# Performance work log

Hardware: AMD Instinct MI355X
Metric: run time of the kernel (lower is better)

The kernel has to match this reference:

```python
import jax, jax.numpy as jnp
import numpy as np

N = 2048      # feature_num (nodes/sensors)
T = 5         # timd_num (window length)
D = 64        # embed_dim
TOPK = 21     # topk + 1 (includes self, cos(i,i)=1)
B = 32        # batch
EPS = 1e-5
NEG_SLOPE = 0.2


def setup_inputs() -> dict:
    key = jax.random.key(0)
    ks = jax.random.split(key, 9)
    s = 1.0 / np.sqrt(D)
    return {
        "x": jax.random.normal(ks[0], (B, N, T), jnp.float32),
        "emb": jax.random.normal(ks[1], (N, D), jnp.float32) * s,      # embedding table
        "W": jax.random.normal(ks[2], (D, T), jnp.float32) * (1.0 / np.sqrt(T)),  # GNN lin weight
        "Wb": jax.random.normal(ks[3], (D,), jnp.float32) * 0.01,       # GNN lin bias
        "a_src": jax.random.normal(ks[4], (2 * D,), jnp.float32) * s,   # attention vec (source half)
        "a_dst": jax.random.normal(ks[5], (2 * D,), jnp.float32) * s,   # attention vec (dest half)
        "gamma": jnp.ones((D,), jnp.float32),                            # BatchNorm1d weight
        "beta": jnp.zeros((D,), jnp.float32),                            # BatchNorm1d bias
        "fc_w": jax.random.normal(ks[6], (1, D), jnp.float32) * s,      # fc weight
        "fc_b": jnp.zeros((1,), jnp.float32),                            # fc bias
    }


def reference(x, emb, W, Wb, a_src, a_dst, gamma, beta, fc_w, fc_b):
    # --- cosine-sim topk graph build ---
    norm = jnp.linalg.norm(emb, axis=-1)                    # [N]
    cos = (emb @ emb.T) / (norm[:, None] * norm[None, :])   # [N,N]
    _, idx = jax.lax.top_k(cos, TOPK)                       # [N,TOPK]
    # scatter one-hot adjacency (vectorized, no per-row loop)
    adj = jnp.zeros((N, N), x.dtype).at[jnp.arange(N)[:, None], idx].set(1.0)
    # --- GNN: GDN-style attention message passing ---
    h = jnp.einsum('bnt,dt->bnd', x, W) + Wb                # [B,N,D]
    g = jnp.concatenate([h, jnp.broadcast_to(emb, h.shape)], axis=-1)  # [B,N,2D]
    e_src = g @ a_src                                       # [B,N]
    e_dst = g @ a_dst                                       # [B,N]
    e = jax.nn.leaky_relu(e_src[:, :, None] + e_dst[:, None, :], NEG_SLOPE)  # [B,N,N]
    e = jnp.where(adj > 0, e, jnp.float32(-1e9))
    alpha = jax.nn.softmax(e, axis=-1)                      # [B,N,N], rows sum to 1 over TOPK nbrs
    z = jax.nn.relu(jnp.einsum('bij,bjd->bid', alpha, h))   # [B,N,D]
    # --- output head: z * emb, BN over channels, relu, fc ---
    out = z * emb                                           # [B,N,D]
    mean = out.mean(axis=(0, 1))                            # BN1d stats over (batch, nodes)
    var = out.var(axis=(0, 1))
    out = (out - mean) * jax.lax.rsqrt(var + EPS) * gamma + beta
    out = jax.nn.relu(out)
    out = out @ fc_w.T + fc_b                               # [B,N,1]
    return out.reshape(-1, N)                               # [B,N]
```

## Files before the change

### kernel.cpp

```cpp
#include <hip/hip_runtime.h>
#include <hip/hip_fp16.h>
#include <math.h>

#define N_NODES 2048
#define T_WIN 5
#define D_EMB 64
#define TOPK 21
#define B_BATCH 32
#define BN_TOTAL (B_BATCH * N_NODES)
#define EPS_BN 1e-5f
#define NEG_SLOPE 0.2f
#define STATS_STRIDE 16

typedef unsigned long long u64;
typedef unsigned short u16;
typedef unsigned int u32;

__device__ __forceinline__ float wave_sum(float v) {
#pragma unroll
    for (int off = 32; off > 0; off >>= 1) v += __shfl_xor(v, off, 64);
    return v;
}

__device__ __forceinline__ u64 max64(u64 a, u64 b) { return a > b ? a : b; }
__device__ __forceinline__ u64 min64(u64 a, u64 b) { return a < b ? a : b; }

__device__ __forceinline__ u64 bitonic_sort64_desc(u64 key, int lane) {
#pragma unroll
    for (int k = 2; k <= 64; k <<= 1) {
#pragma unroll
        for (int j = k >> 1; j >= 1; j >>= 1) {
            u64 pk = __shfl_xor(key, j, 64);
            bool dirDesc = ((lane & k) == 0);
            bool keepMax = (((lane & j) == 0) == dirDesc);
            key = keepMax ? max64(key, pk) : min64(key, pk);
        }
    }
    return key;
}

__device__ __forceinline__ u64 bitonic_merge_top64(u64 a, u64 b, int lane) {
    u64 br = __shfl(b, 63 - lane, 64);
    u64 c = max64(a, br);
#pragma unroll
    for (int j = 32; j >= 1; j >>= 1) {
        u64 pk = __shfl_xor(c, j, 64);
        bool keepMax = ((lane & j) == 0);
        c = keepMax ? max64(c, pk) : min64(c, pk);
    }
    return c;
}

__device__ __forceinline__ u16 f2bf(float f) {
    unsigned u = __float_as_uint(f);
    return (u16)((u + 0x7FFFu + ((u >> 16) & 1u)) >> 16);
}
__device__ __forceinline__ float bf2f(u16 h) {
    return __uint_as_float((unsigned)h << 16);
}

__global__ __launch_bounds__(256) void k_preg(
    const float* __restrict__ x, const float* __restrict__ W,
    const float* __restrict__ Wb, const float* __restrict__ a_src,
    const float* __restrict__ a_dst, const float* __restrict__ emb,
    float* __restrict__ xs2T, float* __restrict__ xd2T,
    float* __restrict__ es_embP, float* __restrict__ ed_embP,
    float* __restrict__ norms, float* __restrict__ dotM,
    float* __restrict__ stats, float* __restrict__ stats2) {
    __shared__ __align__(16) float As[64][68];
    __shared__ __align__(16) float Bs[64][68];
    int t = threadIdx.x;

    if (blockIdx.x >= 528) {
        int eb = blockIdx.x - 528;
        if (eb < 512) {
            if (eb < 2) {
                float* p = eb ? stats2 : stats;
                ((float4*)p)[t] = make_float4(0.f, 0.f, 0.f, 0.f);
            }
            int wid = t >> 6, lane = t & 63;
            int node = eb * 4 + wid;
            float e = emb[node * D_EMB + lane];
            float s2 = wave_sum(e * e);
            float esE = wave_sum(e * a_src[D_EMB + lane]);
            float edE = wave_sum(e * a_dst[D_EMB + lane]);
            if (lane == 0) {
                norms[node] = sqrtf(s2);
                es_embP[node] = esE;
                ed_embP[node] = edE;
            }
        } else {
            __shared__ float cws[5], cwd[5], cbs[2];
            if (t < 12) {
                int which = (t < 5 || t == 10) ? 0 : 1;
                const float* av = which ? a_dst : a_src;
                const float* sp;
                int stride;
                if (t < 10) { int tt = (t < 5) ? t : t - 5; sp = W + tt; stride = T_WIN; }
                else        { sp = Wb; stride = 1; }
                float acc = 0.f;
                for (int d = 0; d < D_EMB; d++) acc += sp[d * stride] * av[d];
                if (t < 5)       cws[t] = acc;
                else if (t < 10) cwd[t - 5] = acc;
                else             cbs[t - 10] = acc;
            }
            __syncthreads();
            float ws0 = cws[0], ws1 = cws[1], ws2 = cws[2], ws3 = cws[3], ws4 = cws[4];
            float wd0 = cwd[0], wd1 = cwd[1], wd2 = cwd[2], wd3 = cwd[3], wd4 = cwd[4];
            float bss = cbs[0], bsd = cbs[1];
            int base = (eb - 512) * 1024;
#pragma unroll
            for (int r = 0; r < 4; r++) {
                int item = base + 256 * r + t;
                const float* xp = x + (size_t)item * T_WIN;
                float x0 = xp[0], x1 = xp[1], x2 = xp[2], x3 = xp[3], x4 = xp[4];
                xs2T[item] = bss + x0 * ws0 + x1 * ws1 + x2 * ws2 + x3 * ws3 + x4 * ws4;
                xd2T[item] = bsd + x0 * wd0 + x1 * wd1 + x2 * wd2 + x3 * wd3 + x4 * wd4;
            }
        }
        return;
    }

    int g = blockIdx.x;
    int a = (int)((sqrtf(8.f * g + 1.f) - 1.f) * 0.5f);
    while ((a + 1) * (a + 2) / 2 <= g) a++;
    while (a * (a + 1) / 2 > g) a--;
    int bq = g - a * (a + 1) / 2;
    int i0 = a * 64, j0 = bq * 64;

    {
        int r = t >> 2, c0 = t & 3;
        const float4* srcA = (const float4*)(emb + (size_t)(i0 + r) * D_EMB);
        const float4* srcB = (const float4*)(emb + (size_t)(j0 + r) * D_EMB);
#pragma unroll
        for (int k = 0; k < 4; k++) {
            int f4 = c0 + 4 * k;
            float4 v = srcA[f4];
            int d = 4 * f4;
            As[d][r] = v.x; As[d + 1][r] = v.y; As[d + 2][r] = v.z; As[d + 3][r] = v.w;
            float4 w = srcB[f4];
            Bs[d][r] = w.x; Bs[d + 1][r] = w.y; Bs[d + 2][r] = w.z; Bs[d + 3][r] = w.w;
        }
    }
    __syncthreads();

    int ti = t & 15, tj = t >> 4;
    float acc[4][4] = {};
#pragma unroll
    for (int d = 0; d < 64; d++) {
        float4 av = *(const float4*)&As[d][4 * ti];
        float4 bv = *(const float4*)&Bs[d][4 * tj];
        acc[0][0] += av.x * bv.x; acc[0][1] += av.x * bv.y; acc[0][2] += av.x * bv.z; acc[0][3] += av.x * bv.w;
        acc[1][0] += av.y * bv.x; acc[1][1] += av.y * bv.y; acc[1][2] += av.y * bv.z; acc[1][3] += av.y * bv.w;
        acc[2][0] += av.z * bv.x; acc[2][1] += av.z * bv.y; acc[2][2] += av.z * bv.z; acc[2][3] += av.z * bv.w;
        acc[3][0] += av.w * bv.x; acc[3][1] += av.w * bv.y; acc[3][2] += av.w * bv.z; acc[3][3] += av.w * bv.w;
    }

#pragma unroll
    for (int r = 0; r < 4; r++) {
        float4 o;
        o.x = acc[r][0]; o.y = acc[r][1]; o.z = acc[r][2]; o.w = acc[r][3];
        int i = i0 + 4 * ti + r;
        *(float4*)(dotM + (size_t)i * N_NODES + j0 + 4 * tj) = o;
        dotM[(size_t)(j0 + 4 * tj + 0) * N_NODES + i] = o.x;
        dotM[(size_t)(j0 + 4 * tj + 1) * N_NODES + i] = o.y;
        dotM[(size_t)(j0 + 4 * tj + 2) * N_NODES + i] = o.z;
        dotM[(size_t)(j0 + 4 * tj + 3) * N_NODES + i] = o.w;
    }
}

__global__ __launch_bounds__(256) void k_select(
    const float* __restrict__ dotM, const float* __restrict__ norms,
    int* __restrict__ idxT) {
    __shared__ u64 candbuf[4][128];
    __shared__ u64 mbuf[2][64];
    int tid = threadIdx.x;
    int wid = tid >> 6, lane = tid & 63;
    int pair = wid >> 1;
    int half = wid & 1;
    int i = blockIdx.x * 2 + pair;
    int jbase = half * (N_NODES / 2);
    const float* row = dotM + (size_t)i * N_NODES + jbase;
    u64* buf = candbuf[wid];
    float ni = norms[i];

    u64 a = 0;
    u64 t = 0;
    int cnt = 0;
    float vcur = row[lane];
    float ncur = norms[jbase + lane];

#pragma unroll 1
    for (int c = 0; c < N_NODES / 128; c++) {
        int j = c * 64 + lane;
        float dv = vcur, nv = ncur;
        if (c < N_NODES / 128 - 1) {
            vcur = row[j + 64];
            ncur = norms[jbase + j + 64];
        }
        float v = dv / (ni * nv);
        unsigned u = __float_as_uint(v);
        u = (u & 0x80000000u) ? ~u : (u | 0x80000000u);
        u64 key = ((u64)u << 32) | (unsigned)(~(j + jbase));
        unsigned long long ball = __ballot(key > t);
        if (ball) {
            int ofs = __popcll(ball & ((1ull << lane) - 1ull));
            if (key > t) buf[cnt + ofs] = key;
            cnt += (int)__popcll(ball);
            if (cnt >= 64) {
                u64 nk = buf[lane];
                nk = bitonic_sort64_desc(nk, lane);
                a = bitonic_merge_top64(a, nk, lane);
                t = __shfl(a, 20, 64);
                int rem = cnt - 64;
                u64 mv = (lane < rem) ? buf[64 + lane] : 0;
                if (lane < rem) buf[lane] = mv;
                cnt = rem;
            }
        }
    }
    while (cnt > 0) {
        int take = cnt < 64 ? cnt : 64;
        u64 nk = (lane < take) ? buf[lane] : 0;
        nk = bitonic_sort64_desc(nk, lane);
        a = bitonic_merge_top64(a, nk, lane);
        t = __shfl(a, 20, 64);
        int rem = cnt - take;
        u64 mv = (lane < rem) ? buf[take + lane] : 0;
        if (lane < rem) buf[lane] = mv;
        cnt = rem;
    }

    if (half) mbuf[pair][lane] = a;
    __syncthreads();
    if (!half) {
        u64 bv = mbuf[pair][lane];
        a = bitonic_merge_top64(a, bv, lane);
        if (lane < TOPK) idxT[lane * N_NODES + i] = (int)(~(unsigned)a);
    }
}

__global__ __launch_bounds__(256) void k_alpha(
    const int* __restrict__ idxT, const float* __restrict__ xs2T,
    const float* __restrict__ xd2T, const float* __restrict__ es_embP,
    const float* __restrict__ ed_embP, u32* __restrict__ paT) {
    __shared__ float sed[N_NODES];
    int g = blockIdx.x;
    int b = g & 31;
    int i0 = (g >> 5) * 256;
    int t = threadIdx.x;

    {
        const float4* sxd = (const float4*)(xd2T + (size_t)b * N_NODES);
        const float4* sde = (const float4*)(ed_embP);
        float4* dst = (float4*)sed;
#pragma unroll
        for (int q = 0; q < 2; q++) {
            int idx = t + 256 * q;
            float4 u = sxd[idx];
            float4 v = sde[idx];
            dst[idx] = make_float4(u.x + v.x, u.y + v.y, u.z + v.z, u.w + v.w);
        }
    }
    __syncthreads();

    int i = i0 + t;
    float es = xs2T[(size_t)b * N_NODES + i] + es_embP[i];
    int jk[TOPK];
    float ev[TOPK];
    float m = -3e38f;
#pragma unroll
    for (int k = 0; k < TOPK; k++) {
        jk[k] = idxT[k * N_NODES + i];
        float e = es + sed[jk[k]];
        e = e > 0.f ? e : NEG_SLOPE * e;
        ev[k] = e;
        m = fmaxf(m, e);
    }
    float s = 0.f;
#pragma unroll
    for (int k = 0; k < TOPK; k++) {
        ev[k] = __expf(ev[k] - m);
        s += ev[k];
    }
    float inv = 1.0f / s;
#pragma unroll
    for (int k = 0; k < TOPK; k++) {
        u16 ah = __half_as_ushort(__float2half_rn(ev[k] * inv));
        paT[((size_t)b * TOPK + k) * N_NODES + i] = ((u32)jk[k] << 16) | (u32)ah;
    }
}

__global__ __launch_bounds__(256, 4) void k_msg(
    const float* __restrict__ x, const float* __restrict__ W,
    const float* __restrict__ Wb, const u32* __restrict__ paT,
    const float* __restrict__ emb, u16* __restrict__ obufT,
    float* __restrict__ stats, float* __restrict__ stats2) {
    __shared__ __align__(16) float hts[N_NODES][4];
    __shared__ float sred[2][4][4];

    int g = blockIdx.x;
    int b = (g & 7) + 8 * ((g >> 3) & 3);
    int c = g >> 5;
    int d0 = c * 4;
    int t = threadIdx.x;
    int wid = t >> 6, lane = t & 63;

    float wc[4][T_WIN], wb4[4];
#pragma unroll
    for (int q = 0; q < 4; q++) {
        wb4[q] = Wb[d0 + q];
#pragma unroll
        for (int tt = 0; tt < T_WIN; tt++) wc[q][tt] = W[(d0 + q) * T_WIN + tt];
    }
    const float* xb = x + (size_t)b * N_NODES * T_WIN;
#pragma unroll
    for (int r = 0; r < 8; r++) {
        int row = t + 256 * r;
        const float* xr = xb + row * T_WIN;
        float x0 = xr[0], x1 = xr[1], x2 = xr[2], x3 = xr[3], x4 = xr[4];
        float h0 = wb4[0] + x0 * wc[0][0] + x1 * wc[0][1] + x2 * wc[0][2] + x3 * wc[0][3] + x4 * wc[0][4];
        float h1 = wb4[1] + x0 * wc[1][0] + x1 * wc[1][1] + x2 * wc[1][2] + x3 * wc[1][3] + x4 * wc[1][4];
        float h2 = wb4[2] + x0 * wc[2][0] + x1 * wc[2][1] + x2 * wc[2][2] + x3 * wc[2][3] + x4 * wc[2][4];
        float h3 = wb4[3] + x0 * wc[3][0] + x1 * wc[3][1] + x2 * wc[3][2] + x3 * wc[3][3] + x4 * wc[3][4];
        *(float4*)&hts[row][0] = make_float4(h0, h1, h2, h3);
    }
    __syncthreads();

    float sacc[4] = {0.f, 0.f, 0.f, 0.f};
    float sacc2[4] = {0.f, 0.f, 0.f, 0.f};
    const u32* pb = paT + (size_t)b * TOPK * N_NODES;
#pragma unroll 1
    for (int r = 0; r < 8; r++) {
        int i = 256 * r + t;
        float4 z = make_float4(0.f, 0.f, 0.f, 0.f);
#pragma unroll
        for (int k = 0; k < TOPK; k++) {
            u32 pa = pb[(size_t)k * N_NODES + i];
            int jk = (int)(pa >> 16);
            float a = __half2float(__ushort_as_half((u16)(pa & 0xFFFFu)));
            float4 h4 = *(const float4*)&hts[jk][0];
            z.x = fmaf(a, h4.x, z.x);
            z.y = fmaf(a, h4.y, z.y);
            z.z = fmaf(a, h4.z, z.z);
            z.w = fmaf(a, h4.w, z.w);
        }
        float4 e4 = *(const float4*)(emb + (size_t)i * D_EMB + d0);
        float4 o;
        o.x = fmaxf(z.x, 0.f) * e4.x;
        o.y = fmaxf(z.y, 0.f) * e4.y;
        o.z = fmaxf(z.z, 0.f) * e4.z;
        o.w = fmaxf(z.w, 0.f) * e4.w;
        ushort4 st;
        st.x = f2bf(o.x); st.y = f2bf(o.y); st.z = f2bf(o.z); st.w = f2bf(o.w);
        ((ushort4*)obufT)[((size_t)c * B_BATCH + b) * N_NODES + i] = st;
        sacc[0] += o.x; sacc[1] += o.y; sacc[2] += o.z; sacc[3] += o.w;
        sacc2[0] += o.x * o.x; sacc2[1] += o.y * o.y;
        sacc2[2] += o.z * o.z; sacc2[3] += o.w * o.w;
    }

#pragma unroll
    for (int q = 0; q < 4; q++) {
        sacc[q] = wave_sum(sacc[q]);
        sacc2[q] = wave_sum(sacc2[q]);
    }
    if (lane == 0) {
#pragma unroll
        for (int q = 0; q < 4; q++) {
            sred[0][wid][q] = sacc[q];
            sred[1][wid][q] = sacc2[q];
        }
    }
    __syncthreads();
    if (t < 8) {
        int q = t & 3, which = t >> 2;
        float v = sred[which][0][q] + sred[which][1][q] + sred[which][2][q] + sred[which][3][q];
        float* dst = which ? stats2 : stats;
        atomicAdd(&dst[(d0 + q) * STATS_STRIDE], v);
    }
}

__global__ __launch_bounds__(256) void k_out(
    const u16* __restrict__ obufT, const float* __restrict__ stats,
    const float* __restrict__ stats2, const float* __restrict__ gamma,
    const float* __restrict__ beta, const float* __restrict__ fc_w,
    const float* __restrict__ fc_b, float* __restrict__ out) {
    __shared__ float smean[64], sinv[64], sg[64], sb[64], sf[64];
    int t = threadIdx.x;
    int g = blockIdx.x;
    int b = g & 31, nc = g >> 5;
    int n = nc * 256 + t;
    const float invM = 1.0f / (float)BN_TOTAL;

    if (t < 64) {
        float mn = stats[t * STATS_STRIDE] * invM;
        float var = stats2[t * STATS_STRIDE] * invM - mn * mn;
        smean[t] = mn;
        sinv[t] = rsqrtf(var + EPS_BN);
        sg[t] = gamma[t]; sb[t] = beta[t]; sf[t] = fc_w[t];
    }
    __syncthreads();

    float fb = fc_b[0];
    float p = 0.f;
#pragma unroll
    for (int c = 0; c < 16; c++) {
        ushort4 h4 = ((const ushort4*)obufT)[((size_t)c * B_BATCH + b) * N_NODES + n];
        float ox = bf2f(h4.x), oy = bf2f(h4.y), oz = bf2f(h4.z), ow = bf2f(h4.w);
        int d = 4 * c;
        float v;
        v = fmaxf((ox - smean[d + 0]) * sinv[d + 0] * sg[d + 0] + sb[d + 0], 0.f); p = fmaf(v, sf[d + 0], p);
        v = fmaxf((oy - smean[d + 1]) * sinv[d + 1] * sg[d + 1] + sb[d + 1], 0.f); p = fmaf(v, sf[d + 1], p);
        v = fmaxf((oz - smean[d + 2]) * sinv[d + 2] * sg[d + 2] + sb[d + 2], 0.f); p = fmaf(v, sf[d + 2], p);
        v = fmaxf((ow - smean[d + 3]) * sinv[d + 3] * sg[d + 3] + sb[d + 3], 0.f); p = fmaf(v, sf[d + 3], p);
    }
    out[b * N_NODES + n] = p + fb;
}

extern "C" void kernel_launch(void* const* d_in, const int* in_sizes, int n_in,
                              void* d_out, int out_size, void* d_ws, size_t ws_size,
                              hipStream_t stream) {
    const float* x     = (const float*)d_in[0];
    const float* emb   = (const float*)d_in[1];
    const float* W     = (const float*)d_in[2];
    const float* Wb    = (const float*)d_in[3];
    const float* a_src = (const float*)d_in[4];
    const float* a_dst = (const float*)d_in[5];
    const float* gamma = (const float*)d_in[6];
    const float* beta  = (const float*)d_in[7];
    const float* fc_w  = (const float*)d_in[8];
    const float* fc_b  = (const float*)d_in[9];
    float* out = (float*)d_out;

    char* ws = (char*)d_ws;
    float* stats   = (float*)(ws + 0);
    float* stats2  = (float*)(ws + 4096);
    int*   idxT    = (int*)  (ws + 8192);
    float* norms   = (float*)(ws + 180224);
    float* es_embP = (float*)(ws + 188416);
    float* ed_embP = (float*)(ws + 196608);
    float* xs2T    = (float*)(ws + 204800);
    float* xd2T    = (float*)(ws + 466944);
    u32*   paT     = (u32*)  (ws + 729088);
    float* dotM    = (float*)(ws + 6234112);
    u16*   obufT   = (u16*)dotM;

    k_preg<<<1104, 256, 0, stream>>>(x, W, Wb, a_src, a_dst, emb,
                                     xs2T, xd2T, es_embP, ed_embP, norms,
                                     dotM, stats, stats2);
    k_select<<<N_NODES / 2, 256, 0, stream>>>(dotM, norms, idxT);
    k_alpha<<<256, 256, 0, stream>>>(idxT, xs2T, xd2T, es_embP, ed_embP, paT);
    k_msg<<<512, 256, 0, stream>>>(x, W, Wb, paT, emb, obufT, stats, stats2);
    k_out<<<256, 256, 0, stream>>>(obufT, stats, stats2, gamma, beta, fc_w, fc_b, out);
}
```

Measured before the change: 127.1 us.

## Store h in fp16 LDS with packed half2 FMA, 8 channels per block

k_msg now stores the projected features h in shared memory as fp16 pairs and accumulates the TOPK-neighbour aggregation with packed half2 FMAs. Each block handles 8 channels instead of 4, and the node range is split into two halves so the grid size stays the same. The intermediate buffer moves to 16-byte uint4 stores and loads, which k_out now reads. This cuts per-block LDS traffic and FMA count but recomputes h for all nodes in both halves, and fp16 accumulation lowers precision.

Result: no change. 126.2 us, median of 2 (-0.7%).

```diff
diff --git a/kernel.cpp b/kernel.cpp
--- a/kernel.cpp
+++ b/kernel.cpp
@@ -294,22 +294,24 @@
 __global__ __launch_bounds__(256, 4) void k_msg(
     const float* __restrict__ x, const float* __restrict__ W,
     const float* __restrict__ Wb, const u32* __restrict__ paT,
-    const float* __restrict__ emb, u16* __restrict__ obufT,
+    const float* __restrict__ emb, uint4* __restrict__ obufT,
     float* __restrict__ stats, float* __restrict__ stats2) {
-    __shared__ __align__(16) float hts[N_NODES][4];
-    __shared__ float sred[2][4][4];
+    __shared__ __align__(16) u32 hts[N_NODES][4];
+    __shared__ float sred[2][4][8];
 
     int g = blockIdx.x;
-    int b = (g & 7) + 8 * ((g >> 3) & 3);
-    int c = g >> 5;
-    int d0 = c * 4;
+    int b = g & 31;
+    int cc = (g >> 5) & 7;
+    int half = g >> 8;
+    int d0 = cc * 8;
+    int ibase = half * (N_NODES / 2);
     int t = threadIdx.x;
     int wid = t >> 6, lane = t & 63;
 
-    float wc[4][T_WIN], wb4[4];
-#pragma unroll
-    for (int q = 0; q < 4; q++) {
-        wb4[q] = Wb[d0 + q];
+    float wc[8][T_WIN], wb8[8];
+#pragma unroll
+    for (int q = 0; q < 8; q++) {
+        wb8[q] = Wb[d0 + q];
 #pragma unroll
         for (int tt = 0; tt < T_WIN; tt++) wc[q][tt] = W[(d0 + q) * T_WIN + tt];
     }
@@ -319,61 +321,82 @@
         int row = t + 256 * r;
         const float* xr = xb + row * T_WIN;
         float x0 = xr[0], x1 = xr[1], x2 = xr[2], x3 = xr[3], x4 = xr[4];
-        float h0 = wb4[0] + x0 * wc[0][0] + x1 * wc[0][1] + x2 * wc[0][2] + x3 * wc[0][3] + x4 * wc[0][4];
-        float h1 = wb4[1] + x0 * wc[1][0] + x1 * wc[1][1] + x2 * wc[1][2] + x3 * wc[1][3] + x4 * wc[1][4];
-        float h2 = wb4[2] + x0 * wc[2][0] + x1 * wc[2][1] + x2 * wc[2][2] + x3 * wc[2][3] + x4 * wc[2][4];
-        float h3 = wb4[3] + x0 * wc[3][0] + x1 * wc[3][1] + x2 * wc[3][2] + x3 * wc[3][3] + x4 * wc[3][4];
-        *(float4*)&hts[row][0] = make_float4(h0, h1, h2, h3);
-    }
-    __syncthreads();
-
-    float sacc[4] = {0.f, 0.f, 0.f, 0.f};
-    float sacc2[4] = {0.f, 0.f, 0.f, 0.f};
+        float h[8];
+#pragma unroll
+        for (int q = 0; q < 8; q++)
+            h[q] = wb8[q] + x0 * wc[q][0] + x1 * wc[q][1] + x2 * wc[q][2]
+                 + x3 * wc[q][3] + x4 * wc[q][4];
+        __half2 p0 = __floats2half2_rn(h[0], h[1]);
+        __half2 p1 = __floats2half2_rn(h[2], h[3]);
+        __half2 p2 = __floats2half2_rn(h[4], h[5]);
+        __half2 p3 = __floats2half2_rn(h[6], h[7]);
+        uint4 sv;
+        sv.x = *(u32*)&p0; sv.y = *(u32*)&p1; sv.z = *(u32*)&p2; sv.w = *(u32*)&p3;
+        *(uint4*)&hts[row][0] = sv;
+    }
+    __syncthreads();
+
+    float sacc[8] = {}, sacc2[8] = {};
     const u32* pb = paT + (size_t)b * TOPK * N_NODES;
 #pragma unroll 1
-    for (int r = 0; r < 8; r++) {
-        int i = 256 * r + t;
-        float4 z = make_float4(0.f, 0.f, 0.f, 0.f);
+    for (int r = 0; r < 4; r++) {
+        int i = ibase + 256 * r + t;
+        __half2 z01 = __floats2half2_rn(0.f, 0.f);
+        __half2 z23 = z01, z45 = z01, z67 = z01;
 #pragma unroll
         for (int k = 0; k < TOPK; k++) {
             u32 pa = pb[(size_t)k * N_NODES + i];
             int jk = (int)(pa >> 16);
-            float a = __half2float(__ushort_as_half((u16)(pa & 0xFFFFu)));
-            float4 h4 = *(const float4*)&hts[jk][0];
-            z.x = fmaf(a, h4.x, z.x);
-            z.y = fmaf(a, h4.y, z.y);
-            z.z = fmaf(a, h4.z, z.z);
-            z.w = fmaf(a, h4.w, z.w);
-        }
-        float4 e4 = *(const float4*)(emb + (size_t)i * D_EMB + d0);
-        float4 o;
-        o.x = fmaxf(z.x, 0.f) * e4.x;
-        o.y = fmaxf(z.y, 0.f) * e4.y;
-        o.z = fmaxf(z.z, 0.f) * e4.z;
-        o.w = fmaxf(z.w, 0.f) * e4.w;
-        ushort4 st;
-        st.x = f2bf(o.x); st.y = f2bf(o.y); st.z = f2bf(o.z); st.w = f2bf(o.w);
-        ((ushort4*)obufT)[((size_t)c * B_BATCH + b) * N_NODES + i] = st;
-        sacc[0] += o.x; sacc[1] += o.y; sacc[2] += o.z; sacc[3] += o.w;
-        sacc2[0] += o.x * o.x; sacc2[1] += o.y * o.y;
-        sacc2[2] += o.z * o.z; sacc2[3] += o.w * o.w;
-    }
-
-#pragma unroll
-    for (int q = 0; q < 4; q++) {
+            __half2 av = __half2half2(__ushort_as_half((u16)(pa & 0xFFFFu)));
+            uint4 hv = *(const uint4*)&hts[jk][0];
+            z01 = __hfma2(av, *(__half2*)&hv.x, z01);
+            z23 = __hfma2(av, *(__half2*)&hv.y, z23);
+            z45 = __hfma2(av, *(__half2*)&hv.z, z45);
+            z67 = __hfma2(av, *(__half2*)&hv.w, z67);
+        }
+        float2 f01 = __half22float2(z01);
+        float2 f23 = __half22float2(z23);
+        float2 f45 = __half22float2(z45);
+        float2 f67 = __half22float2(z67);
+        float4 e0 = *(const float4*)(emb + (size_t)i * D_EMB + d0);
+        float4 e1 = *(const float4*)(emb + (size_t)i * D_EMB + d0 + 4);
+        float o[8];
+        o[0] = fmaxf(f01.x, 0.f) * e0.x;
+        o[1] = fmaxf(f01.y, 0.f) * e0.y;
+        o[2] = fmaxf(f23.x, 0.f) * e0.z;
+        o[3] = fmaxf(f23.y, 0.f) * e0.w;
+        o[4] = fmaxf(f45.x, 0.f) * e1.x;
+        o[5] = fmaxf(f45.y, 0.f) * e1.y;
+        o[6] = fmaxf(f67.x, 0.f) * e1.z;
+        o[7] = fmaxf(f67.y, 0.f) * e1.w;
+        uint4 st;
+        st.x = (u32)f2bf(o[0]) | ((u32)f2bf(o[1]) << 16);
+        st.y = (u32)f2bf(o[2]) | ((u32)f2bf(o[3]) << 16);
+        st.z = (u32)f2bf(o[4]) | ((u32)f2bf(o[5]) << 16);
+        st.w = (u32)f2bf(o[6]) | ((u32)f2bf(o[7]) << 16);
+        obufT[((size_t)cc * B_BATCH + b) * N_NODES + i] = st;
+#pragma unroll
+        for (int q = 0; q < 8; q++) {
+            sacc[q] += o[q];
+            sacc2[q] += o[q] * o[q];
+        }
+    }
+
+#pragma unroll
+    for (int q = 0; q < 8; q++) {
         sacc[q] = wave_sum(sacc[q]);
         sacc2[q] = wave_sum(sacc2[q]);
     }
     if (lane == 0) {
 #pragma unroll
-        for (int q = 0; q < 4; q++) {
+        for (int q = 0; q < 8; q++) {
             sred[0][wid][q] = sacc[q];
             sred[1][wid][q] = sacc2[q];
         }
     }
     __syncthreads();
-    if (t < 8) {
-        int q = t & 3, which = t >> 2;
+    if (t < 16) {
+        int q = t & 7, which = t >> 3;
         float v = sred[which][0][q] + sred[which][1][q] + sred[which][2][q] + sred[which][3][q];
         float* dst = which ? stats2 : stats;
         atomicAdd(&dst[(d0 + q) * STATS_STRIDE], v);
@@ -381,7 +404,7 @@
 }
 
 __global__ __launch_bounds__(256) void k_out(
-    const u16* __restrict__ obufT, const float* __restrict__ stats,
+    const uint4* __restrict__ obufT, const float* __restrict__ stats,
     const float* __restrict__ stats2, const float* __restrict__ gamma,
     const float* __restrict__ beta, const float* __restrict__ fc_w,
     const float* __restrict__ fc_b, float* __restrict__ out) {
@@ -404,15 +427,19 @@
     float fb = fc_b[0];
     float p = 0.f;
 #pragma unroll
-    for (int c = 0; c < 16; c++) {
-        ushort4 h4 = ((const ushort4*)obufT)[((size_t)c * B_BATCH + b) * N_NODES + n];
-        float ox = bf2f(h4.x), oy = bf2f(h4.y), oz = bf2f(h4.z), ow = bf2f(h4.w);
-        int d = 4 * c;
-        float v;
-        v = fmaxf((ox - smean[d + 0]) * sinv[d + 0] * sg[d + 0] + sb[d + 0], 0.f); p = fmaf(v, sf[d + 0], p);
-        v = fmaxf((oy - smean[d + 1]) * sinv[d + 1] * sg[d + 1] + sb[d + 1], 0.f); p = fmaf(v, sf[d + 1], p);
-        v = fmaxf((oz - smean[d + 2]) * sinv[d + 2] * sg[d + 2] + sb[d + 2], 0.f); p = fmaf(v, sf[d + 2], p);
-        v = fmaxf((ow - smean[d + 3]) * sinv[d + 3] * sg[d + 3] + sb[d + 3], 0.f); p = fmaf(v, sf[d + 3], p);
+    for (int cc = 0; cc < 8; cc++) {
+        uint4 hv = obufT[((size_t)cc * B_BATCH + b) * N_NODES + n];
+        int d = cc * 8;
+        float o[8];
+        o[0] = bf2f((u16)(hv.x & 0xFFFFu)); o[1] = bf2f((u16)(hv.x >> 16));
+        o[2] = bf2f((u16)(hv.y & 0xFFFFu)); o[3] = bf2f((u16)(hv.y >> 16));
+        o[4] = bf2f((u16)(hv.z & 0xFFFFu)); o[5] = bf2f((u16)(hv.z >> 16));
+        o[6] = bf2f((u16)(hv.w & 0xFFFFu)); o[7] = bf2f((u16)(hv.w >> 16));
+#pragma unroll
+        for (int q = 0; q < 8; q++) {
+            float v = fmaxf((o[q] - smean[d + q]) * sinv[d + q] * sg[d + q] + sb[d + q], 0.f);
+            p = fmaf(v, sf[d + q], p);
+        }
     }
     out[b * N_NODES + n] = p + fb;
 }
@@ -443,7 +470,7 @@
     float* xd2T    = (float*)(ws + 466944);
     u32*   paT     = (u32*)  (ws + 729088);
     float* dotM    = (float*)(ws + 6234112);
-    u16*   obufT   = (u16*)dotM;
+    uint4* obufT   = (uint4*)dotM;
 
     k_preg<<<1104, 256, 0, stream>>>(x, W, Wb, a_src, a_dst, emb,
                                      xs2T, xd2T, es_embP, ed_embP, norms,
```
